# Kernel tuning notes

Hardware: AMD Instinct MI355X
Metric: run time of the kernel (lower is better)

Reference implementation:

```python
import jax, jax.numpy as jnp
import numpy as np

B, T, C, H = 2, 2048, 1024, 16
D = C // H
HID = 4 * C
EPS = 1e-5


def _rmsnorm(x, w):
    return w * (x * jax.lax.rsqrt(jnp.mean(x * x, axis=-1, keepdims=True) + EPS))


def setup_inputs() -> dict:
    key = jax.random.key(0)
    ks = jax.random.split(key, 12)
    s = 0.02
    inp = {
        "x": jax.random.normal(ks[0], (B, T, C), jnp.float32),
        "mask": jnp.tril(jnp.ones((T, T), jnp.int32))[None, None],  # (1,1,T,T) causal
        "attn_norm_w": jnp.ones((C,), jnp.float32),
        "mlp_norm_w": jnp.ones((C,), jnp.float32),
        "q_w": jax.random.normal(ks[1], (C, C), jnp.float32) * s,
        "q_b": jnp.zeros((C,), jnp.float32),
        "k_w": jax.random.normal(ks[2], (C, C), jnp.float32) * s,
        "k_b": jnp.zeros((C,), jnp.float32),
        "v_w": jax.random.normal(ks[3], (C, C), jnp.float32) * s,
        "v_b": jnp.zeros((C,), jnp.float32),
        "o_w": jax.random.normal(ks[4], (C, C), jnp.float32) * s,
        "o_b": jnp.zeros((C,), jnp.float32),
        "w1": jax.random.normal(ks[5], (C, HID), jnp.float32) * s,
        "b1": jnp.zeros((HID,), jnp.float32),
        "w2": jax.random.normal(ks[6], (HID, C), jnp.float32) * s,
        "b2": jnp.zeros((C,), jnp.float32),
    }
    return inp


def reference(x, mask, attn_norm_w, mlp_norm_w, q_w, q_b, k_w, k_b, v_w, v_b,
              o_w, o_b, w1, b1, w2, b2):
    # Pre-norm path (use_post_norm=False)
    h = _rmsnorm(x, attn_norm_w)
    q = (h @ q_w + q_b).reshape(B, T, H, D).transpose(0, 2, 1, 3)  # (B,H,T,D)
    k = (h @ k_w + k_b).reshape(B, T, H, D).transpose(0, 2, 1, 3)
    v = (h @ v_w + v_b).reshape(B, T, H, D).transpose(0, 2, 1, 3)
    scores = jnp.einsum("bhqd,bhkd->bhqk", q, k) / jnp.sqrt(jnp.float32(D))
    scores = jnp.where(mask == 0, jnp.float32(-jnp.inf), scores)
    attn = jax.nn.softmax(scores, axis=-1)  # (B,H,T,T)
    ctx = jnp.einsum("bhqk,bhkd->bhqd", attn, v)
    attn_out = ctx.transpose(0, 2, 1, 3).reshape(B, T, C) @ o_w + o_b
    x = x + attn_out
    m = _rmsnorm(x, mlp_norm_w)
    mlp_out = jax.nn.gelu(m @ w1 + b1, approximate=False) @ w2 + b2
    x = x + mlp_out
    return (x, k, v)
```

## Files before the change

kernel.cpp:

```cpp
#include <hip/hip_runtime.h>
#include <hip/hip_bf16.h>


#define B_ 2
#define T_ 2048
#define C_ 1024
#define H_ 16
#define D_ 64
#define HID_ 4096
#define M_ 4096

typedef __bf16 bf16x8 __attribute__((ext_vector_type(8)));
typedef float f32x4 __attribute__((ext_vector_type(4)));
using bf16 = __hip_bfloat16;

static __device__ __forceinline__ f32x4 mfma16(bf16x8 a, bf16x8 b, f32x4 c) {
  return __builtin_amdgcn_mfma_f32_16x16x32_bf16(a, b, c, 0, 0, 0);
}

static __device__ __forceinline__ void gload16(const bf16* g, bf16* l) {
  __builtin_amdgcn_global_load_lds(
      (const __attribute__((address_space(1))) unsigned int*)g,
      (__attribute__((address_space(3))) unsigned int*)l, 16, 0, 0);
}

static __device__ __forceinline__ unsigned short bfbits(float x) {
  __hip_bfloat16 h = __float2bfloat16(x);
  return *(unsigned short*)&h;
}

__global__ __launch_bounds__(256) void cvt_transpose(const float* __restrict__ in,
                                                     bf16* __restrict__ out, int K, int N) {
  __shared__ float tile[32][33];
  int tid = threadIdx.x, tx = tid & 31, ty = tid >> 5;
  int n0 = blockIdx.x * 32, k0 = blockIdx.y * 32;
#pragma unroll
  for (int i = 0; i < 4; ++i) {
    int r = ty + i * 8;
    tile[r][tx] = in[(size_t)(k0 + r) * N + n0 + tx];
  }
  __syncthreads();
#pragma unroll
  for (int i = 0; i < 4; ++i) {
    int r = ty + i * 8;
    out[(size_t)(n0 + r) * K + k0 + tx] = __float2bfloat16(tile[tx][r]);
  }
}

__global__ __launch_bounds__(256) void pack_bias(const float* __restrict__ q,
                                                 const float* __restrict__ k,
                                                 const float* __restrict__ v,
                                                 float* __restrict__ o) {
  int i = blockIdx.x * 256 + threadIdx.x;
  o[i] = i < 1024 ? q[i] : (i < 2048 ? k[i - 1024] : v[i - 2048]);
}

__global__ __launch_bounds__(256) void rmsnorm_kernel(const float* __restrict__ x,
                                                      const float* __restrict__ w,
                                                      bf16* __restrict__ out) {
  int row = blockIdx.x, tid = threadIdx.x;
  float4 v = ((const float4*)(x + (size_t)row * C_))[tid];
  float ss = v.x * v.x + v.y * v.y + v.z * v.z + v.w * v.w;
#pragma unroll
  for (int d = 1; d < 64; d <<= 1) ss += __shfl_xor(ss, d);
  __shared__ float wsum[4];
  if ((tid & 63) == 0) wsum[tid >> 6] = ss;
  __syncthreads();
  float tot = wsum[0] + wsum[1] + wsum[2] + wsum[3];
  float r = rsqrtf(tot * (1.0f / C_) + 1e-5f);
  float4 wv = ((const float4*)w)[tid];
  bf16* o = out + (size_t)row * C_ + tid * 4;
  o[0] = __float2bfloat16(v.x * wv.x * r);
  o[1] = __float2bfloat16(v.y * wv.y * r);
  o[2] = __float2bfloat16(v.z * wv.z * r);
  o[3] = __float2bfloat16(v.w * wv.w * r);
}

__global__ __launch_bounds__(256) void addp_kernel(float* __restrict__ out,
                                                   const float* __restrict__ p, int n4) {
  int i = blockIdx.x * 256 + threadIdx.x;
  int stride = gridDim.x * 256;
  for (; i < n4; i += stride) {
    float4 a = ((const float4*)out)[i];
    float4 b = ((const float4*)p)[i];
    a.x += b.x; a.y += b.y; a.z += b.z; a.w += b.w;
    ((float4*)out)[i] = a;
  }
}

template <int EPI>
__global__ __launch_bounds__(512, 2) void gemm256_kernel(
    const bf16* __restrict__ A, const bf16* __restrict__ Bt, const float* __restrict__ bias,
    bf16* __restrict__ bfout, float* __restrict__ fout, bf16* __restrict__ vtb,
    int M, int N, int K) {
  __shared__ bf16 As[2][256 * 64];
  __shared__ bf16 Bs[2][256 * 64];
  int tid = threadIdx.x, wid = tid >> 6, l = tid & 63, g = l >> 4, c = l & 15;
  int wm = wid >> 2, wn = wid & 3;
  int nwg = gridDim.x * gridDim.y;
  int bidl = blockIdx.y * gridDim.x + blockIdx.x;
  int wgid = (bidl & 7) * (nwg >> 3) + (bidl >> 3);
  int bx = wgid % gridDim.x, by = wgid / gridDim.x;
  int m0 = by * 256, n0 = bx * 256;
  int NT = K >> 6;
  int srow = l >> 3;
  int sgr = (l & 7) ^ srow;

  auto stage = [&](int t, int buf) {
#pragma unroll
    for (int j = 0; j < 4; ++j) {
      int q = (wid << 2) + j;
      gload16(A + (size_t)(m0 + q * 8 + srow) * K + t * 64 + sgr * 8, &As[buf][q * 512]);
      gload16(Bt + (size_t)(n0 + q * 8 + srow) * K + t * 64 + sgr * 8, &Bs[buf][q * 512]);
    }
  };

  f32x4 acc[8][4] = {};
  stage(0, 0);
  __syncthreads();
  for (int t = 0; t < NT; ++t) {
    int cur = t & 1;
    if (t + 1 < NT) stage(t + 1, cur ^ 1);
#pragma unroll
    for (int kk = 0; kk < 2; ++kk) {
      bf16x8 bfr[4];
#pragma unroll
      for (int nf = 0; nf < 4; ++nf) {
        int row = wn * 64 + nf * 16 + c;
        bfr[nf] = *(const bf16x8*)&Bs[cur][row * 64 + (((kk * 4 + g) ^ (c & 7)) << 3)];
      }
#pragma unroll
      for (int mf = 0; mf < 8; ++mf) {
        int row = wm * 128 + mf * 16 + c;
        bf16x8 af = *(const bf16x8*)&As[cur][row * 64 + (((kk * 4 + g) ^ (c & 7)) << 3)];
#pragma unroll
        for (int nf = 0; nf < 4; ++nf) acc[mf][nf] = mfma16(af, bfr[nf], acc[mf][nf]);
      }
    }
    __syncthreads();
  }

#pragma unroll
  for (int mf = 0; mf < 8; ++mf) {
#pragma unroll
    for (int nf = 0; nf < 4; ++nf) {
      int gn = n0 + wn * 64 + nf * 16 + c;
      float bv = bias[gn];
#pragma unroll
      for (int r = 0; r < 4; ++r) {
        int gm = m0 + wm * 128 + mf * 16 + g * 4 + r;
        float v = acc[mf][nf][r] + bv;
        if (EPI == 0) {
          int part = gn >> 10, wi = gn & 1023, hh = wi >> 6, d = wi & 63;
          int b_ = gm >> 11, t = gm & 2047;
          size_t idx = ((size_t)(b_ * H_ + hh) * T_ + t) * D_ + d;
          if (part == 2) {
            vtb[((size_t)(b_ * H_ + hh) * D_ + d) * T_ + t] = __float2bfloat16(v);
            fout[(size_t)2 * 4194304 + idx] = v;
          } else {
            bfout[(size_t)part * 4194304 + idx] = __float2bfloat16(v);
            if (part) fout[(size_t)part * 4194304 + idx] = v;
          }
        } else {
          float gl = 0.5f * v * (1.0f + erff(v * 0.70710678118f));
          bfout[(size_t)gm * N + gn] = __float2bfloat16(gl);
        }
      }
    }
  }
}

template <int EPI, int DBUF, int SK>
__global__ __launch_bounds__(256) void gemm_kernel(
    const bf16* __restrict__ A, const bf16* __restrict__ Bt, const float* __restrict__ bias,
    bf16* __restrict__ bfout, float* __restrict__ fout, const float* __restrict__ res,
    float* __restrict__ paux, int M, int N, int K) {
  __shared__ bf16 Al[(DBUF ? 2 : 1) * 128 * 64];
  __shared__ bf16 Bl[(DBUF ? 2 : 1) * 128 * 64];
  int tid = threadIdx.x, w = tid >> 6, l = tid & 63;
  int g = l >> 4, c = l & 15;
  int nwg = gridDim.x * gridDim.y;
  int bidl = blockIdx.y * gridDim.x + blockIdx.x;
  int wgid = (bidl & 7) * (nwg >> 3) + (bidl >> 3);
  int bx = wgid % gridDim.x, by = wgid / gridDim.x;
  int m0 = by * 128, n0 = bx * 128;
  int wm = (w >> 1) * 64, wn = (w & 1) * 64;
  int Kc = K / SK;
  int kbase = (SK > 1) ? (int)blockIdx.z * Kc : 0;
  int KT = Kc >> 6;
  int lrow = l >> 3, lcol = (l & 7) * 8;

  const bf16* gA = A + (size_t)(m0 + w * 32 + lrow) * K + kbase + lcol;
  const bf16* gB = Bt + (size_t)(n0 + w * 32 + lrow) * K + kbase + lcol;

  auto stage = [&](int kt, int buf) {
#pragma unroll
    for (int i = 0; i < 4; ++i) {
      gload16(gA + (size_t)i * 8 * K + kt * 64, Al + buf * 8192 + (w * 4 + i) * 512);
      gload16(gB + (size_t)i * 8 * K + kt * 64, Bl + buf * 8192 + (w * 4 + i) * 512);
    }
  };
  auto compute = [&](int buf, f32x4 (&acc)[4][4]) {
#pragma unroll
    for (int ch = 0; ch < 2; ++ch) {
      bf16x8 af[4], bfr[4];
#pragma unroll
      for (int f = 0; f < 4; ++f)
        af[f] = *(const bf16x8*)&Al[buf * 8192 + (wm + f * 16 + c) * 64 + ch * 32 + g * 8];
#pragma unroll
      for (int f = 0; f < 4; ++f)
        bfr[f] = *(const bf16x8*)&Bl[buf * 8192 + (wn + f * 16 + c) * 64 + ch * 32 + g * 8];
#pragma unroll
      for (int mf = 0; mf < 4; ++mf)
#pragma unroll
        for (int nf = 0; nf < 4; ++nf) acc[mf][nf] = mfma16(af[mf], bfr[nf], acc[mf][nf]);
    }
  };

  f32x4 acc[4][4] = {};
  if (DBUF) {
    stage(0, 0);
    __syncthreads();
    for (int kt = 0; kt < KT; ++kt) {
      int cur = kt & 1;
      if (kt + 1 < KT) stage(kt + 1, cur ^ 1);
      compute(cur, acc);
      __syncthreads();
    }
  } else {
    for (int kt = 0; kt < KT; ++kt) {
      stage(kt, 0);
      __syncthreads();
      compute(0, acc);
      __syncthreads();
    }
  }

#pragma unroll
  for (int mf = 0; mf < 4; ++mf) {
#pragma unroll
    for (int nf = 0; nf < 4; ++nf) {
      int gn = n0 + wn + nf * 16 + c;
      float bv = bias ? bias[gn] : 0.f;
#pragma unroll
      for (int r = 0; r < 4; ++r) {
        int gm = m0 + wm + mf * 16 + g * 4 + r;
        float vr = acc[mf][nf][r];
        float v = vr + bv;
        if (SK > 1 && blockIdx.z > 0) {
          paux[(size_t)gm * N + gn] = vr;
        } else if (EPI == 1) {
          size_t idx = (size_t)gm * N + gn;
          fout[idx] = v + res[idx];
        } else {
          size_t idx = (size_t)gm * N + gn;
          float gl = 0.5f * v * (1.0f + erff(v * 0.70710678118f));
          bfout[idx] = __float2bfloat16(gl);
        }
      }
    }
  }
}

__global__ __launch_bounds__(256, 2) void attn_kernel(const bf16* __restrict__ Q,
                                                      const bf16* __restrict__ Kb,
                                                      const bf16* __restrict__ Vt,
                                                      bf16* __restrict__ ctx) {
  constexpr int LDP = 72;
  __shared__ bf16 Kl[2][64 * 64];
  __shared__ bf16 Vl[2][64 * 64];
  __shared__ bf16 Pl[4][2][16 * LDP];
  __shared__ float alw[4][2][16];
  int tid = threadIdx.x, w = tid >> 6, l = tid & 63, g = l >> 4, c = l & 15;
  int bid = blockIdx.x;
  int qt = 15 - (bid >> 5);
  int bh = bid & 31;
  int qbase = qt * 128 + w * 32;
  const bf16* Qh = Q + (size_t)bh * T_ * D_;
  const bf16* Kh = Kb + (size_t)bh * T_ * D_;
  const bf16* Vh = Vt + (size_t)bh * T_ * D_;

  int srow = l >> 3;
  int sce = ((l & 7) * 8) ^ (srow << 3);
  int cswz = (c & 7) << 3;

  auto stage = [&](int ti, int buf) {
#pragma unroll
    for (int i = 0; i < 2; ++i) {
      int row = i * 32 + w * 8 + srow;
      gload16(&Kh[(size_t)(ti * 64 + row) * D_ + sce], &Kl[buf][i * 2048 + w * 512]);
      gload16(&Vh[(size_t)row * T_ + ti * 64 + sce], &Vl[buf][i * 2048 + w * 512]);
    }
  };

  int NT = 2 * qt + 2;
  stage(0, 0);

  bf16x8 aq[2][2];
#pragma unroll
  for (int qf = 0; qf < 2; ++qf)
#pragma unroll
    for (int ch = 0; ch < 2; ++ch)
      aq[qf][ch] = *(const bf16x8*)&Qh[(size_t)(qbase + qf * 16 + c) * D_ + ch * 32 + g * 8];

  f32x4 o[2][4] = {};
  float mrun[2] = {-1e30f, -1e30f};
  float lrun[2] = {0.f, 0.f};

  __syncthreads();

  for (int ti = 0; ti < NT; ++ti) {
    int cur = ti & 1;
    int kv0 = ti * 64;
    if (ti + 1 < NT) stage(ti + 1, cur ^ 1);

    f32x4 sf[2][4];
#pragma unroll
    for (int kb = 0; kb < 4; ++kb) {
      bf16x8 bk0 = *(const bf16x8*)&Kl[cur][(kb * 16 + c) * 64 + ((g * 8) ^ cswz)];
      bf16x8 bk1 = *(const bf16x8*)&Kl[cur][(kb * 16 + c) * 64 + ((32 + g * 8) ^ cswz)];
#pragma unroll
      for (int qf = 0; qf < 2; ++qf) {
        f32x4 t = {};
        t = mfma16(bk0, aq[qf][0], t);
        t = mfma16(bk1, aq[qf][1], t);
        sf[qf][kb] = t;
      }
    }

    float s[2][4][4];
#pragma unroll
    for (int qf = 0; qf < 2; ++qf)
#pragma unroll
      for (int kb = 0; kb < 4; ++kb)
#pragma unroll
        for (int r = 0; r < 4; ++r) s[qf][kb][r] = sf[qf][kb][r] * 0.125f;
    if (kv0 + 63 > qbase) {
#pragma unroll
      for (int qf = 0; qf < 2; ++qf)
#pragma unroll
        for (int kb = 0; kb < 4; ++kb)
#pragma unroll
          for (int r = 0; r < 4; ++r) {
            int qi = qbase + qf * 16 + c;
            int kv = kv0 + kb * 16 + g * 4 + r;
            if (kv > qi) s[qf][kb][r] = -1e30f;
          }
    }

#pragma unroll
    for (int qf = 0; qf < 2; ++qf) {
      float m01 = fmaxf(fmaxf(s[qf][0][0], s[qf][0][1]), fmaxf(s[qf][0][2], s[qf][0][3]));
      float m23 = fmaxf(fmaxf(s[qf][1][0], s[qf][1][1]), fmaxf(s[qf][1][2], s[qf][1][3]));
      float m45 = fmaxf(fmaxf(s[qf][2][0], s[qf][2][1]), fmaxf(s[qf][2][2], s[qf][2][3]));
      float m67 = fmaxf(fmaxf(s[qf][3][0], s[qf][3][1]), fmaxf(s[qf][3][2], s[qf][3][3]));
      float tm = fmaxf(fmaxf(m01, m23), fmaxf(m45, m67));
      tm = fmaxf(tm, __shfl_xor(tm, 16));
      tm = fmaxf(tm, __shfl_xor(tm, 32));
      float mn = fmaxf(mrun[qf], tm);
      float al = __expf(mrun[qf] - mn);
      mrun[qf] = mn;
      float asum = 0.f;
#pragma unroll
      for (int kb = 0; kb < 4; ++kb)
#pragma unroll
        for (int r = 0; r < 4; ++r) {
          float pv = __expf(s[qf][kb][r] - mn);
          s[qf][kb][r] = pv;
          asum += pv;
        }
      asum += __shfl_xor(asum, 16);
      asum += __shfl_xor(asum, 32);
      lrun[qf] = lrun[qf] * al + asum;
      if (l < 16) alw[w][qf][c] = al;
    }

#pragma unroll
    for (int qf = 0; qf < 2; ++qf)
#pragma unroll
      for (int kb = 0; kb < 4; ++kb) {
        union { unsigned short u[4]; uint2 v2; } pk;
#pragma unroll
        for (int r = 0; r < 4; ++r) pk.u[r] = bfbits(s[qf][kb][r]);
        *(uint2*)&Pl[w][qf][c * LDP + kb * 16 + g * 4] = pk.v2;
      }

#pragma unroll
    for (int qf = 0; qf < 2; ++qf) {
      f32x4 a4 = *(const f32x4*)&alw[w][qf][g * 4];
#pragma unroll
      for (int db = 0; db < 4; ++db)
#pragma unroll
        for (int r = 0; r < 4; ++r) o[qf][db][r] *= a4[r];
    }

    bf16x8 bvv[4][2];
#pragma unroll
    for (int db = 0; db < 4; ++db)
#pragma unroll
      for (int ck = 0; ck < 2; ++ck)
        bvv[db][ck] = *(const bf16x8*)&Vl[cur][(db * 16 + c) * 64 + ((ck * 32 + g * 8) ^ cswz)];

#pragma unroll
    for (int qf = 0; qf < 2; ++qf) {
      bf16x8 pa0 = *(const bf16x8*)&Pl[w][qf][c * LDP + g * 8];
      bf16x8 pa1 = *(const bf16x8*)&Pl[w][qf][c * LDP + 32 + g * 8];
#pragma unroll
      for (int db = 0; db < 4; ++db) {
        o[qf][db] = mfma16(pa0, bvv[db][0], o[qf][db]);
        o[qf][db] = mfma16(pa1, bvv[db][1], o[qf][db]);
      }
    }
    __syncthreads();
  }

#pragma unroll
  for (int qf = 0; qf < 2; ++qf)
    if (l < 16) alw[w][qf][c] = 1.0f / lrun[qf];
  int b_ = bh >> 4, hh = bh & 15;
#pragma unroll
  for (int qf = 0; qf < 2; ++qf) {
    f32x4 i4 = *(const f32x4*)&alw[w][qf][g * 4];
#pragma unroll
    for (int r = 0; r < 4; ++r)
#pragma unroll
      for (int db = 0; db < 4; ++db)
        ctx[(size_t)(b_ * T_ + qbase + qf * 16 + g * 4 + r) * C_ + hh * D_ + db * 16 + c] =
            __float2bfloat16(o[qf][db][r] * i4[r]);
  }
}

extern "C" void kernel_launch(void* const* d_in, const int* in_sizes, int n_in, void* d_out,
                              int out_size, void* d_ws, size_t ws_size, hipStream_t stream) {
  const float* x = (const float*)d_in[0];
  const float* anw = (const float*)d_in[2];
  const float* mnw = (const float*)d_in[3];
  const float* q_w = (const float*)d_in[4];
  const float* q_b = (const float*)d_in[5];
  const float* k_w = (const float*)d_in[6];
  const float* k_b = (const float*)d_in[7];
  const float* v_w = (const float*)d_in[8];
  const float* v_b = (const float*)d_in[9];
  const float* o_w = (const float*)d_in[10];
  const float* o_b = (const float*)d_in[11];
  const float* w1 = (const float*)d_in[12];
  const float* b1 = (const float*)d_in[13];
  const float* w2 = (const float*)d_in[14];
  const float* b2 = (const float*)d_in[15];
  float* out = (float*)d_out;
  char* ws = (char*)d_ws;

  bf16* qkvT = (bf16*)(ws + 0);
  bf16* owT = (bf16*)(ws + 6291456);
  bf16* w1T = (bf16*)(ws + 8388608);
  bf16* w2T = (bf16*)(ws + 16777216);
  bf16* h = (bf16*)(ws + 25165824);
  bf16* qb = (bf16*)(ws + 33554432);
  bf16* kb = (bf16*)(ws + 41943040);
  bf16* vtb = (bf16*)(ws + 58720256);
  bf16* ctx = (bf16*)(ws + 67108864);
  float* x2 = (float*)(ws + 33554432);
  bf16* m = h;
  bf16* hid = (bf16*)(ws + 50331648);
  float* qkvb = (float*)(ws + 75497472);
  float* p1 = (float*)(ws + 0);

  cvt_transpose<<<dim3(32, 32), 256, 0, stream>>>(q_w, qkvT, 1024, 1024);
  cvt_transpose<<<dim3(32, 32), 256, 0, stream>>>(k_w, qkvT + 1048576, 1024, 1024);
  cvt_transpose<<<dim3(32, 32), 256, 0, stream>>>(v_w, qkvT + 2097152, 1024, 1024);
  cvt_transpose<<<dim3(32, 32), 256, 0, stream>>>(o_w, owT, 1024, 1024);
  cvt_transpose<<<dim3(128, 32), 256, 0, stream>>>(w1, w1T, 1024, 4096);
  cvt_transpose<<<dim3(32, 128), 256, 0, stream>>>(w2, w2T, 4096, 1024);
  pack_bias<<<12, 256, 0, stream>>>(q_b, k_b, v_b, qkvb);

  rmsnorm_kernel<<<4096, 256, 0, stream>>>(x, anw, h);

  gemm256_kernel<0><<<dim3(12, 16), 512, 0, stream>>>(h, qkvT, qkvb, qb, out, vtb,
                                                      4096, 3072, 1024);

  attn_kernel<<<512, 256, 0, stream>>>(qb, kb, vtb, ctx);

  gemm_kernel<1, 1, 1><<<dim3(8, 32), 256, 0, stream>>>(ctx, owT, o_b, nullptr, x2, x,
                                                        nullptr, 4096, 1024, 1024);

  rmsnorm_kernel<<<4096, 256, 0, stream>>>(x2, mnw, m);

  gemm256_kernel<2><<<dim3(16, 16), 512, 0, stream>>>(m, w1T, b1, hid, nullptr, nullptr,
                                                      4096, 4096, 1024);
  gemm_kernel<1, 1, 2><<<dim3(8, 32, 2), 256, 0, stream>>>(hid, w2T, b2, nullptr, out, x2,
                                                           p1, 4096, 1024, 4096);
  addp_kernel<<<2048, 256, 0, stream>>>(out, p1, 1048576);
}
```

Baseline: 309.3 us.

## Overlap next-tile loads with compute via partial vmcnt waits and XOR-swizzled LDS

Replaces the full __syncthreads in both double-buffered GEMM loops with an explicit s_waitcnt vmcnt(8) plus s_barrier. The wait lets the next tile's global-to-LDS loads stay in flight while the current tile is computed, and s_setprio raises wave priority during the MFMA section. The 128x128 GEMM also switches to XOR-swizzled LDS addressing, matching the 256 kernel, to cut bank conflicts. The risk is that correctness now depends on the exact vmcnt count matching the number of loads issued per stage.

```diff
diff --git a/kernel.cpp b/kernel.cpp
--- a/kernel.cpp
+++ b/kernel.cpp
@@ -13,6 +13,9 @@
 typedef __bf16 bf16x8 __attribute__((ext_vector_type(8)));
 typedef float f32x4 __attribute__((ext_vector_type(4)));
 using bf16 = __hip_bfloat16;
+
+#define WAIT_VM(N) asm volatile("s_waitcnt vmcnt(" #N ")" ::: "memory")
+#define SBAR() asm volatile("s_barrier" ::: "memory")
 
 static __device__ __forceinline__ f32x4 mfma16(bf16x8 a, bf16x8 b, f32x4 c) {
   return __builtin_amdgcn_mfma_f32_16x16x32_bf16(a, b, c, 0, 0, 0);
@@ -117,10 +120,16 @@
 
   f32x4 acc[8][4] = {};
   stage(0, 0);
-  __syncthreads();
   for (int t = 0; t < NT; ++t) {
     int cur = t & 1;
-    if (t + 1 < NT) stage(t + 1, cur ^ 1);
+    if (t + 1 < NT) {
+      stage(t + 1, cur ^ 1);
+      WAIT_VM(8);
+    } else {
+      WAIT_VM(0);
+    }
+    SBAR();
+    __builtin_amdgcn_s_setprio(1);
 #pragma unroll
     for (int kk = 0; kk < 2; ++kk) {
       bf16x8 bfr[4];
@@ -137,7 +146,9 @@
         for (int nf = 0; nf < 4; ++nf) acc[mf][nf] = mfma16(af, bfr[nf], acc[mf][nf]);
       }
     }
-    __syncthreads();
+    __builtin_amdgcn_s_setprio(0);
+    __builtin_amdgcn_sched_barrier(0);
+    SBAR();
   }
 
 #pragma unroll
@@ -188,10 +199,11 @@
   int Kc = K / SK;
   int kbase = (SK > 1) ? (int)blockIdx.z * Kc : 0;
   int KT = Kc >> 6;
-  int lrow = l >> 3, lcol = (l & 7) * 8;
-
-  const bf16* gA = A + (size_t)(m0 + w * 32 + lrow) * K + kbase + lcol;
-  const bf16* gB = Bt + (size_t)(n0 + w * 32 + lrow) * K + kbase + lcol;
+  int lrow = l >> 3;
+  int sgr = (l & 7) ^ lrow;
+
+  const bf16* gA = A + (size_t)(m0 + w * 32 + lrow) * K + kbase + sgr * 8;
+  const bf16* gB = Bt + (size_t)(n0 + w * 32 + lrow) * K + kbase + sgr * 8;
 
   auto stage = [&](int kt, int buf) {
 #pragma unroll
@@ -206,10 +218,12 @@
       bf16x8 af[4], bfr[4];
 #pragma unroll
       for (int f = 0; f < 4; ++f)
-        af[f] = *(const bf16x8*)&Al[buf * 8192 + (wm + f * 16 + c) * 64 + ch * 32 + g * 8];
+        af[f] = *(const bf16x8*)&Al[buf * 8192 + (wm + f * 16 + c) * 64 +
+                                    (((ch * 4 + g) ^ (c & 7)) << 3)];
 #pragma unroll
       for (int f = 0; f < 4; ++f)
-        bfr[f] = *(const bf16x8*)&Bl[buf * 8192 + (wn + f * 16 + c) * 64 + ch * 32 + g * 8];
+        bfr[f] = *(const bf16x8*)&Bl[buf * 8192 + (wn + f * 16 + c) * 64 +
+                                     (((ch * 4 + g) ^ (c & 7)) << 3)];
 #pragma unroll
       for (int mf = 0; mf < 4; ++mf)
 #pragma unroll
@@ -220,12 +234,20 @@
   f32x4 acc[4][4] = {};
   if (DBUF) {
     stage(0, 0);
-    __syncthreads();
     for (int kt = 0; kt < KT; ++kt) {
       int cur = kt & 1;
-      if (kt + 1 < KT) stage(kt + 1, cur ^ 1);
+      if (kt + 1 < KT) {
+        stage(kt + 1, cur ^ 1);
+        WAIT_VM(8);
+      } else {
+        WAIT_VM(0);
+      }
+      SBAR();
+      __builtin_amdgcn_s_setprio(1);
       compute(cur, acc);
-      __syncthreads();
+      __builtin_amdgcn_s_setprio(0);
+      __builtin_amdgcn_sched_barrier(0);
+      SBAR();
     }
   } else {
     for (int kt = 0; kt < KT; ++kt) {
```

New measurement: 299.9 us. 3.0% less time.
